# Kernel optimization log

Measured on AMD Instinct MI355X. Metric: run time of the kernel, lower is better.

## Reference

```python
import jax, jax.numpy as jnp
import numpy as np

B, N, K = 4, 4096, 16
DP, DM = 64, 128
EPS = 1e-8


def setup_inputs() -> dict:
    key = jax.random.key(0)
    ks = jax.random.split(key, 32)
    g = lambda i, shape, fan: jax.random.normal(ks[i], shape, jnp.float32) / np.sqrt(fan)
    inp = {
        'xyz': jax.random.normal(ks[0], (B, N, 3), jnp.float32),
        'features': jax.random.normal(ks[1], (B, N, DP), jnp.float32),
        # fc1: d_points -> d_model
        'fc1_w': g(2, (DP, DM), DP), 'fc1_b': jnp.zeros((DM,), jnp.float32),
        # fc2: d_model -> d_points
        'fc2_w': g(3, (DM, DP), DM), 'fc2_b': jnp.zeros((DP,), jnp.float32),
        # fc_delta: Linear(3,DM) -> ReLU -> Linear(DM,DM)
        'd1_w': g(4, (3, DM), 3), 'd1_b': jnp.zeros((DM,), jnp.float32),
        'd2_w': g(5, (DM, DM), DM), 'd2_b': jnp.zeros((DM,), jnp.float32),
        # fc_gamma: Linear(DM,DM) -> ReLU -> Linear(DM,DM)
        'g1_w': g(6, (DM, DM), DM), 'g1_b': jnp.zeros((DM,), jnp.float32),
        'g2_w': g(7, (DM, DM), DM), 'g2_b': jnp.zeros((DM,), jnp.float32),
        # q/k/v projections, no bias
        'wq_w': g(8, (DM, DM), DM), 'wk_w': g(9, (DM, DM), DM), 'wv_w': g(10, (DM, DM), DM),
        # fc_sim: Linear(DM+1, DM)
        'sim_w': g(11, (DM + 1, DM), DM + 1), 'sim_b': jnp.zeros((DM,), jnp.float32),
    }
    return inp


def _gather(t, idx):
    # t: [B, N, C], idx: [B, N, K] -> [B, N, K, C]
    bidx = jnp.arange(t.shape[0])[:, None, None]
    return t[bidx, idx]


def reference(xyz, features, fc1_w, fc1_b, fc2_w, fc2_b, d1_w, d1_b, d2_w, d2_b,
              g1_w, g1_b, g2_w, g2_b, wq_w, wk_w, wv_w, sim_w, sim_b):
    # pairwise squared distances [B, N, N]
    sq = jnp.sum(xyz * xyz, axis=-1)
    dists = sq[:, :, None] + sq[:, None, :] - 2.0 * jnp.einsum('bnc,bmc->bnm', xyz, xyz)
    knn_idx = jnp.argsort(dists, axis=-1)[:, :, :K]            # [B, N, K]

    knn_xyz = _gather(xyz, knn_idx)                            # [B, N, K, 3]
    x = features @ fc1_w + fc1_b                               # [B, N, DM]
    q = x @ wq_w                                               # [B, N, DM]
    k = _gather(x @ wk_w, knn_idx)                             # [B, N, K, DM]
    v = _gather(x @ wv_w, knn_idx)                             # [B, N, K, DM]

    rel_pos = xyz[:, :, None, :] - knn_xyz                     # [B, N, K, 3]
    pos_enc = jax.nn.relu(rel_pos @ d1_w + d1_b) @ d2_w + d2_b # [B, N, K, DM]

    qe = q[:, :, None, :]                                      # [B, N, 1, DM]
    # torch cosine_similarity: dot / (max(||q||,eps) * max(||k||,eps))
    qn = jnp.maximum(jnp.linalg.norm(q, axis=-1), EPS)[:, :, None]
    kn = jnp.maximum(jnp.linalg.norm(k, axis=-1), EPS)
    sim = jnp.sum(qe * k, axis=-1) / (qn * kn)                 # [B, N, K]

    rel_qk = jnp.concatenate([sim[..., None], qe - k], axis=-1)  # [B, N, K, DM+1]
    rel_qk = rel_qk @ sim_w + sim_b                            # [B, N, K, DM]

    attn = jax.nn.relu((rel_qk + pos_enc) @ g1_w + g1_b) @ g2_w + g2_b
    attn = jax.nn.softmax(attn / np.sqrt(DM).astype(np.float32), axis=-2)  # over K

    res = jnp.einsum('bnkf,bnkf->bnf', attn, v + pos_enc)      # [B, N, DM]
    res = res @ fc2_w + fc2_b + features                       # [B, N, DP]
    return res, attn
```

## Files before the change

### kernel.cpp

```cpp
#include <hip/hip_runtime.h>
#include <hip/hip_bf16.h>

#define BB 4
#define NN 4096
#define KK 16
#define DP 64
#define DM 128
#define DMP 132
#define SPITCH 264
#define EPSF 1e-8f
#define OUT0N ((size_t)BB * NN * DP)

typedef unsigned short u16t;
typedef __attribute__((ext_vector_type(8))) short s8v;
typedef __attribute__((ext_vector_type(4))) float f4v;

__device__ int g_flag;

__device__ __forceinline__ float u2f(u16t u) {
    unsigned int x = ((unsigned int)u) << 16;
    return __uint_as_float(x);
}
__device__ __forceinline__ u16t f2u(float v) {
    __hip_bfloat16 h = __float2bfloat16(v);
    return *(u16t*)&h;
}
__device__ __forceinline__ void splitf(float x, u16t& h, u16t& l) {
    const unsigned xb = __float_as_uint(x);
    h = (u16t)(xb >> 16);
    const float hf = __uint_as_float(xb & 0xffff0000u);
    l = (u16t)(__float_as_uint(x - hf) >> 16);
}

template<int DT> struct IO;
template<> struct IO<0> {
    static __device__ __forceinline__ float ld(const void* p, size_t i) { return ((const float*)p)[i]; }
    static __device__ __forceinline__ void ld4(const void* p, size_t i, float o[4]) {
        float4 v = *(const float4*)((const float*)p + i);
        o[0] = v.x; o[1] = v.y; o[2] = v.z; o[3] = v.w;
    }
    static __device__ __forceinline__ void st(void* p, size_t i, float v) { ((float*)p)[i] = v; }
};
template<> struct IO<1> {
    static __device__ __forceinline__ float ld(const void* p, size_t i) { return u2f(((const u16t*)p)[i]); }
    static __device__ __forceinline__ void ld4(const void* p, size_t i, float o[4]) {
        ushort4 v = *(const ushort4*)((const u16t*)p + i);
        o[0] = u2f(v.x); o[1] = u2f(v.y); o[2] = u2f(v.z); o[3] = u2f(v.w);
    }
    static __device__ __forceinline__ void st(void* p, size_t i, float v) { ((u16t*)p)[i] = f2u(v); }
};

__global__ __launch_bounds__(64) void detect_kernel(const void* feat) {
    const int tid = threadIdx.x;
    float x = u2f(((const u16t*)feat)[2 * tid]);
    float a = fabsf(x);
    bool sane = (x == 0.0f) || (a > 1e-4f && a < 50.0f);
    unsigned long long m = __ballot(sane);
    if (tid == 0) g_flag = (__popcll(m) >= 32) ? 1 : 0;
}

struct QkvSmem { float sf[DP]; float sx[DM]; };

template<int DT>
__device__ __forceinline__ void qkv_body(QkvSmem& s,
    const void* feat, const void* fc1_w, const void* fc1_b,
    const void* wq, const void* wk, const void* wv,
    float* __restrict__ qbuf, float* __restrict__ kbuf, float* __restrict__ vbuf)
{
    const int bn = blockIdx.x;
    const int tid = threadIdx.x;
    if (tid < DP) s.sf[tid] = IO<DT>::ld(feat, (size_t)bn * DP + tid);
    __syncthreads();
    float x = IO<DT>::ld(fc1_b, tid);
#pragma unroll 4
    for (int i = 0; i < DP; i++) x = fmaf(s.sf[i], IO<DT>::ld(fc1_w, i * DM + tid), x);
    s.sx[tid] = x;
    __syncthreads();
    float q = 0.f, k = 0.f, v = 0.f;
    for (int i0 = 0; i0 < DM; i0 += 4) {
        float4 xv = *(const float4*)&s.sx[i0];
        const float xs[4] = { xv.x, xv.y, xv.z, xv.w };
#pragma unroll
        for (int j = 0; j < 4; j++) {
            q = fmaf(xs[j], IO<DT>::ld(wq, (i0 + j) * DM + tid), q);
            k = fmaf(xs[j], IO<DT>::ld(wk, (i0 + j) * DM + tid), k);
            v = fmaf(xs[j], IO<DT>::ld(wv, (i0 + j) * DM + tid), v);
        }
    }
    qbuf[(size_t)bn * DM + tid] = q;
    kbuf[(size_t)bn * DM + tid] = k;
    vbuf[(size_t)bn * DM + tid] = v;
}

__global__ __launch_bounds__(128) void qkv_kernel(
    const void* feat, const void* fc1_w, const void* fc1_b,
    const void* wq, const void* wk, const void* wv,
    float* qbuf, float* kbuf, float* vbuf)
{
    __shared__ __align__(16) QkvSmem s;
    if (g_flag) qkv_body<1>(s, feat, fc1_w, fc1_b, wq, wk, wv, qbuf, kbuf, vbuf);
    else        qkv_body<0>(s, feat, fc1_w, fc1_b, wq, wk, wv, qbuf, kbuf, vbuf);
}

struct Qkv16Smem { float sf[16][DP]; float sx[16][DMP]; };

template<int DT>
__device__ __forceinline__ void qkv16_body(Qkv16Smem& s,
    const void* feat, const void* fc1_w, const void* fc1_b,
    const void* wq, const void* wk, const void* wv,
    float* __restrict__ qbuf, float* __restrict__ kbuf, float* __restrict__ vbuf)
{
    const int pnt0 = blockIdx.x << 4;
    const int tid = threadIdx.x;
    {
        const int r = tid >> 4, c4 = (tid & 15) << 2;
        float o[4];
        IO<DT>::ld4(feat, (size_t)(pnt0 + r) * DP + c4, o);
        s.sf[r][c4 + 0] = o[0]; s.sf[r][c4 + 1] = o[1];
        s.sf[r][c4 + 2] = o[2]; s.sf[r][c4 + 3] = o[3];
    }
    __syncthreads();
    const int c = tid & 127, h = tid >> 7;
    {
        float acc[8];
        const float fb = IO<DT>::ld(fc1_b, c);
#pragma unroll
        for (int pp = 0; pp < 8; pp++) acc[pp] = fb;
        for (int i = 0; i < DP; i++) {
            const float w = IO<DT>::ld(fc1_w, (size_t)i * DM + c);
#pragma unroll
            for (int pp = 0; pp < 8; pp++) acc[pp] = fmaf(s.sf[h * 8 + pp][i], w, acc[pp]);
        }
#pragma unroll
        for (int pp = 0; pp < 8; pp++) s.sx[h * 8 + pp][c] = acc[pp];
    }
    __syncthreads();
    {
        float aq[8], ak[8], av[8];
#pragma unroll
        for (int pp = 0; pp < 8; pp++) { aq[pp] = 0.f; ak[pp] = 0.f; av[pp] = 0.f; }
        for (int i0 = 0; i0 < DM; i0 += 4) {
            float x4[8][4];
#pragma unroll
            for (int pp = 0; pp < 8; pp++) {
                const float4 xv = *(const float4*)&s.sx[h * 8 + pp][i0];
                x4[pp][0] = xv.x; x4[pp][1] = xv.y; x4[pp][2] = xv.z; x4[pp][3] = xv.w;
            }
#pragma unroll
            for (int j = 0; j < 4; j++) {
                const float wqv = IO<DT>::ld(wq, (size_t)(i0 + j) * DM + c);
                const float wkv = IO<DT>::ld(wk, (size_t)(i0 + j) * DM + c);
                const float wvv = IO<DT>::ld(wv, (size_t)(i0 + j) * DM + c);
#pragma unroll
                for (int pp = 0; pp < 8; pp++) {
                    aq[pp] = fmaf(x4[pp][j], wqv, aq[pp]);
                    ak[pp] = fmaf(x4[pp][j], wkv, ak[pp]);
                    av[pp] = fmaf(x4[pp][j], wvv, av[pp]);
                }
            }
        }
#pragma unroll
        for (int pp = 0; pp < 8; pp++) {
            const size_t row = (size_t)(pnt0 + h * 8 + pp) * DM + c;
            qbuf[row] = aq[pp]; kbuf[row] = ak[pp]; vbuf[row] = av[pp];
        }
    }
}

__global__ __launch_bounds__(256) void qkv16_kernel(
    const void* feat, const void* fc1_w, const void* fc1_b,
    const void* wq, const void* wk, const void* wv,
    float* qbuf, float* kbuf, float* vbuf)
{
    __shared__ __align__(16) Qkv16Smem s;
    if (g_flag) qkv16_body<1>(s, feat, fc1_w, fc1_b, wq, wk, wv, qbuf, kbuf, vbuf);
    else        qkv16_body<0>(s, feat, fc1_w, fc1_b, wq, wk, wv, qbuf, kbuf, vbuf);
}

template<int DT>
__device__ __forceinline__ void knn_body(float4* __restrict__ sc,
    const void* xyz, int* dst, int dstride, void* dout, int in_out)
{
    if (in_out) {
        if (DT) { dst = (int*)((u16t*)dout + OUT0N); dstride = (KK * DM) / 2; }
        else    { dst = (int*)((float*)dout + OUT0N); dstride = KK * DM; }
    }
    const int b = blockIdx.x >> 9;
    const int tid = threadIdx.x;
    for (int j = tid; j < NN; j += 512) {
        float x = IO<DT>::ld(xyz, ((size_t)b * NN + j) * 3 + 0);
        float y = IO<DT>::ld(xyz, ((size_t)b * NN + j) * 3 + 1);
        float z = IO<DT>::ld(xyz, ((size_t)b * NN + j) * 3 + 2);
        float sq = __fadd_rn(__fadd_rn(__fmul_rn(x, x), __fmul_rn(y, y)), __fmul_rn(z, z));
        sc[j] = make_float4(x, y, z, sq);
    }
    __syncthreads();
    const int lane = tid & 63;
    const int wave = tid >> 6;
    const int r = ((blockIdx.x & 511) << 3) + wave;
    const float4 qc = sc[r];

    float d[KK];
    int id[KK];
#pragma unroll
    for (int t = 0; t < KK; t++) { d[t] = 3.4e38f; id[t] = 0x7fffffff; }

    for (int j = lane; j < NN; j += 64) {
        const float4 c = sc[j];
        const float dot = __fadd_rn(__fadd_rn(__fmul_rn(qc.x, c.x), __fmul_rn(qc.y, c.y)),
                                    __fmul_rn(qc.z, c.z));
        const float dist = __fsub_rn(__fadd_rn(qc.w, c.w), __fmul_rn(2.0f, dot));
        if (dist < d[KK - 1]) {
            float cd = dist; int ci = j;
#pragma unroll
            for (int t = 0; t < KK; t++) {
                const bool sw = (cd < d[t]);
                const float od = d[t]; const int oi = id[t];
                d[t]  = sw ? cd : d[t];
                id[t] = sw ? ci : id[t];
                cd = sw ? od : cd;
                ci = sw ? oi : ci;
            }
        }
    }

    const size_t base = (size_t)(b * NN + r) * (size_t)dstride;
#pragma unroll
    for (int t = 0; t < KK; t++) {
        float bd = d[0]; int bi = id[0];
#pragma unroll
        for (int off = 32; off >= 1; off >>= 1) {
            const float od = __shfl_xor(bd, off, 64);
            const int   oi = __shfl_xor(bi, off, 64);
            if (od < bd || (od == bd && oi < bi)) { bd = od; bi = oi; }
        }
        const bool win = (d[0] == bd) && (id[0] == bi);
        if (win) {
#pragma unroll
            for (int u = 0; u < KK - 1; u++) { d[u] = d[u + 1]; id[u] = id[u + 1]; }
            d[KK - 1] = 3.4e38f; id[KK - 1] = 0x7fffffff;
        }
        if (lane == t) dst[base + t] = bi;
    }
}

__global__ __launch_bounds__(512) void knn_kernel(
    const void* xyz, int* dst, int dstride, void* dout, int in_out)
{
    __shared__ __align__(16) float4 sc[NN];
    if (g_flag) knn_body<1>(sc, xyz, dst, dstride, dout, in_out);
    else        knn_body<0>(sc, xyz, dst, dstride, dout, in_out);
}

template<int DT>
__device__ __forceinline__ void gemm_tile(const float* __restrict__ IN,
                                          const void* __restrict__ W, int woff,
                                          int kg, int f0, float acc[4][4])
{
#pragma unroll
    for (int a = 0; a < 4; a++)
#pragma unroll
        for (int c = 0; c < 4; c++) acc[a][c] = 0.f;
    for (int i0 = 0; i0 < DM; i0 += 4) {
        float w[4][4];
#pragma unroll
        for (int j = 0; j < 4; j++) IO<DT>::ld4(W, (size_t)woff + (i0 + j) * DM + f0, w[j]);
#pragma unroll
        for (int kk = 0; kk < 4; kk++) {
            float4 x4 = *(const float4*)(IN + (kg * 4 + kk) * DMP + i0);
            const float xs[4] = { x4.x, x4.y, x4.z, x4.w };
#pragma unroll
            for (int ff = 0; ff < 4; ff++)
#pragma unroll
                for (int j = 0; j < 4; j++)
                    acc[kk][ff] = fmaf(xs[j], w[j][ff], acc[kk][ff]);
        }
    }
}

template<int DT>
__device__ __forceinline__ void wprep_body(const void* sim_w, const void* d2_w,
                                           const void* g1_w, const void* g2_w,
                                           u16t* __restrict__ wprep)
{
    const int m  = blockIdx.x >> 3;
    const int t  = blockIdx.x & 7;
    const int ks = threadIdx.x >> 6;
    const int lane = threadIdx.x & 63;
    const void* src = (m == 0) ? sim_w : (m == 1) ? d2_w : (m == 2) ? g1_w : g2_w;
    const int srcoff = (m == 0) ? DM : 0;
    u16t* hi = wprep + (size_t)m * 32768;
    u16t* lo = hi + 16384;
    const int c  = t * 16 + (lane & 15);
    const int k0 = ks * 32 + ((lane >> 4) << 3);
    s8v vh, vl;
#pragma unroll
    for (int j = 0; j < 8; j++) {
        const float x = IO<DT>::ld(src, (size_t)srcoff + (size_t)(k0 + j) * DM + c);
        const u16t h = f2u(x);
        vh[j] = (short)h;
        vl[j] = (short)f2u(x - u2f(h));
    }
    const size_t off = ((size_t)(t * 4 + ks) * 64 + lane) * 8;
    *(s8v*)(hi + off) = vh;
    *(s8v*)(lo + off) = vl;
}

__global__ __launch_bounds__(256) void wprep_kernel(
    const void* sim_w, const void* d2_w, const void* g1_w, const void* g2_w,
    u16t* wprep)
{
    if (g_flag) wprep_body<1>(sim_w, d2_w, g1_w, g2_w, wprep);
    else        wprep_body<0>(sim_w, d2_w, g1_w, g2_w, wprep);
}

__device__ __forceinline__ void mfma_g(const u16t* __restrict__ SP,
                                       const u16t* __restrict__ wmat,
                                       int lane, int w, f4v acc[4][2])
{
    const u16t* whi = wmat;
    const u16t* wlo = wmat + 16384;
    const int arow = lane & 15;
    const int ak   = (lane >> 4) << 3;
#pragma unroll
    for (int ks = 0; ks < 4; ks++) {
        const size_t o0 = ((size_t)(((2 * w + 0) * 4 + ks) * 64) + lane) * 8;
        const size_t o1 = ((size_t)(((2 * w + 1) * 4 + ks) * 64) + lane) * 8;
        const s8v b0h = *(const s8v*)(whi + o0);
        const s8v b0l = *(const s8v*)(wlo + o0);
        const s8v b1h = *(const s8v*)(whi + o1);
        const s8v b1l = *(const s8v*)(wlo + o1);
#pragma unroll
        for (int m = 0; m < 4; m++) {
            const u16t* ar = SP + (size_t)(m * 16 + arow) * SPITCH + ak + ks * 32;
            const s8v ah = *(const s8v*)ar;
            const s8v al = *(const s8v*)(ar + 128);
            acc[m][0] = __builtin_amdgcn_mfma_f32_16x16x32_bf16(ah, b0h, acc[m][0], 0, 0, 0);
            acc[m][0] = __builtin_amdgcn_mfma_f32_16x16x32_bf16(ah, b0l, acc[m][0], 0, 0, 0);
            acc[m][0] = __builtin_amdgcn_mfma_f32_16x16x32_bf16(al, b0h, acc[m][0], 0, 0, 0);
            acc[m][1] = __builtin_amdgcn_mfma_f32_16x16x32_bf16(ah, b1h, acc[m][1], 0, 0, 0);
            acc[m][1] = __builtin_amdgcn_mfma_f32_16x16x32_bf16(ah, b1l, acc[m][1], 0, 0, 0);
            acc[m][1] = __builtin_amdgcn_mfma_f32_16x16x32_bf16(al, b1h, acc[m][1], 0, 0, 0);
        }
    }
}

struct Attn4Smem {
    u16t  SP[64 * SPITCH];
    float sq[4][DM];
    float sres[4][DM];
    float ssim[64];
    float srp[64][3];
    int   sidx[64];
};

template<int DT>
__device__ __forceinline__ void attn4w_body(Attn4Smem& s,
    const void* xyz, const void* feat,
    const void* fc2_w, const void* fc2_b,
    const void* d1_w, const void* d1_b, const void* d2_b,
    const void* g1_b, const void* g2_b,
    const void* sim_w, const void* sim_b,
    const float* __restrict__ qbuf, const float* __restrict__ kbuf,
    const float* __restrict__ vbuf,
    const int* __restrict__ knn, const u16t* __restrict__ wprep, void* dout)
{
    void* out0 = dout;
    void* out1 = DT ? (void*)((u16t*)dout + OUT0N) : (void*)((float*)dout + OUT0N);
    const int pnt0 = blockIdx.x << 2;
    const int b = pnt0 >> 12;
    const int tid = threadIdx.x;
    const int lane = tid & 63;
    const int w = tid >> 6;
    const int h = lane >> 4;
    const int c = lane & 15;

    if (tid < 64) {
        int sv = knn[(size_t)(pnt0 + (tid >> 4)) * KK + (tid & 15)];
        sv = (sv < 0) ? 0 : (sv > NN - 1 ? NN - 1 : sv);
        s.sidx[tid] = sv;
        const int pt = tid >> 4;
        const int grow = (b << 12) + sv;
#pragma unroll
        for (int c3 = 0; c3 < 3; c3++)
            s.srp[tid][c3] = IO<DT>::ld(xyz, (size_t)(pnt0 + pt) * 3 + c3)
                           - IO<DT>::ld(xyz, (size_t)grow * 3 + c3);
    }
    const float2 q2 = *(const float2*)&qbuf[(size_t)(pnt0 + w) * DM + lane * 2];
    *(float2*)&s.sq[w][lane * 2] = q2;
    float qq = fmaf(q2.x, q2.x, q2.y * q2.y);
#pragma unroll
    for (int off = 1; off <= 32; off <<= 1) qq += __shfl_xor(qq, off, 64);
    const float qn = fmaxf(sqrtf(qq), EPSF);
    __syncthreads();

    {
        const int row = tid >> 2, cb = (tid & 3) << 5;
        const float rx = s.srp[row][0], ry = s.srp[row][1], rz = s.srp[row][2];
        u16t* hp = &s.SP[row * SPITCH];
#pragma unroll
        for (int j4 = 0; j4 < 32; j4 += 4) {
            float w0[4], w1[4], w2[4], bb[4];
            IO<DT>::ld4(d1_w, (size_t)0 * DM + cb + j4, w0);
            IO<DT>::ld4(d1_w, (size_t)1 * DM + cb + j4, w1);
            IO<DT>::ld4(d1_w, (size_t)2 * DM + cb + j4, w2);
            IO<DT>::ld4(d1_b, cb + j4, bb);
            ushort4 hv, lv;
#pragma unroll
            for (int jj = 0; jj < 4; jj++) {
                const float hx = fmaxf(fmaf(rz, w2[jj], fmaf(ry, w1[jj], fmaf(rx, w0[jj], bb[jj]))), 0.f);
                u16t hs, ls; splitf(hx, hs, ls);
                ((u16t*)&hv)[jj] = hs; ((u16t*)&lv)[jj] = ls;
            }
            *(ushort4*)(hp + cb + j4) = hv;
            *(ushort4*)(hp + 128 + cb + j4) = lv;
        }
    }
    __syncthreads();

    f4v pe[4][2] = { { {0,0,0,0},{0,0,0,0} }, { {0,0,0,0},{0,0,0,0} },
                     { {0,0,0,0},{0,0,0,0} }, { {0,0,0,0},{0,0,0,0} } };
    mfma_g(s.SP, wprep + 1 * 32768, lane, w, pe);
#pragma unroll
    for (int nt = 0; nt < 2; nt++) {
        const float bv = IO<DT>::ld(d2_b, (2 * w + nt) * 16 + c);
#pragma unroll
        for (int m = 0; m < 4; m++)
#pragma unroll
            for (int r = 0; r < 4; r++) pe[m][nt][r] += bv;
    }
    __syncthreads();

    {
        const int row = tid >> 2, cb = (tid & 3) << 5;
        const int pt = row >> 4;
        const int grow = (b << 12) + s.sidx[row];
        const float* krow = &kbuf[(size_t)grow * DM];
        u16t* hp = &s.SP[row * SPITCH];
        float sk = 0.f, sd = 0.f;
#pragma unroll
        for (int j4 = 0; j4 < 32; j4 += 4) {
            const float4 kv = *(const float4*)&krow[cb + j4];
            const float4 qv = *(const float4*)&s.sq[pt][cb + j4];
            ushort4 hv, lv;
            splitf(qv.x - kv.x, hv.x, lv.x);
            splitf(qv.y - kv.y, hv.y, lv.y);
            splitf(qv.z - kv.z, hv.z, lv.z);
            splitf(qv.w - kv.w, hv.w, lv.w);
            *(ushort4*)(hp + cb + j4) = hv;
            *(ushort4*)(hp + 128 + cb + j4) = lv;
            sk = fmaf(kv.x, kv.x, fmaf(kv.y, kv.y, fmaf(kv.z, kv.z, fmaf(kv.w, kv.w, sk))));
            sd = fmaf(qv.x, kv.x, fmaf(qv.y, kv.y, fmaf(qv.z, kv.z, fmaf(qv.w, kv.w, sd))));
        }
        sk += __shfl_xor(sk, 1, 64); sk += __shfl_xor(sk, 2, 64);
        sd += __shfl_xor(sd, 1, 64); sd += __shfl_xor(sd, 2, 64);
        if ((tid & 3) == 0) {
            const float kn = fmaxf(sqrtf(sk), EPSF);
            s.ssim[row] = sd / (qn * kn);
        }
    }
    __syncthreads();

    {
        f4v a1[4][2] = { { {0,0,0,0},{0,0,0,0} }, { {0,0,0,0},{0,0,0,0} },
                         { {0,0,0,0},{0,0,0,0} }, { {0,0,0,0},{0,0,0,0} } };
        mfma_g(s.SP, wprep + 0 * 32768, lane, w, a1);
        __syncthreads();
#pragma unroll
        for (int nt = 0; nt < 2; nt++) {
            const int col = (2 * w + nt) * 16 + c;
            const float bv  = IO<DT>::ld(sim_b, col);
            const float w0v = IO<DT>::ld(sim_w, col);
#pragma unroll
            for (int m = 0; m < 4; m++)
#pragma unroll
                for (int r = 0; r < 4; r++) {
                    const int row = m * 16 + 4 * h + r;
                    const float val = a1[m][nt][r] + bv + s.ssim[row] * w0v + pe[m][nt][r];
                    u16t hs, ls; splitf(val, hs, ls);
                    s.SP[(size_t)row * SPITCH + col] = hs;
                    s.SP[(size_t)row * SPITCH + 128 + col] = ls;
                }
        }
    }
    __syncthreads();

    {
        f4v a3[4][2] = { { {0,0,0,0},{0,0,0,0} }, { {0,0,0,0},{0,0,0,0} },
                         { {0,0,0,0},{0,0,0,0} }, { {0,0,0,0},{0,0,0,0} } };
        mfma_g(s.SP, wprep + 2 * 32768, lane, w, a3);
        __syncthreads();
#pragma unroll
        for (int nt = 0; nt < 2; nt++) {
            const int col = (2 * w + nt) * 16 + c;
            const float bv = IO<DT>::ld(g1_b, col);
#pragma unroll
            for (int m = 0; m < 4; m++)
#pragma unroll
                for (int r = 0; r < 4; r++) {
                    const int row = m * 16 + 4 * h + r;
                    const float val = fmaxf(a3[m][nt][r] + bv, 0.f);
                    u16t hs, ls; splitf(val, hs, ls);
                    s.SP[(size_t)row * SPITCH + col] = hs;
                    s.SP[(size_t)row * SPITCH + 128 + col] = ls;
                }
        }
    }
    __syncthreads();

    f4v av[4][2];
    {
        f4v a4[4][2] = { { {0,0,0,0},{0,0,0,0} }, { {0,0,0,0},{0,0,0,0} },
                         { {0,0,0,0},{0,0,0,0} }, { {0,0,0,0},{0,0,0,0} } };
        mfma_g(s.SP, wprep + 3 * 32768, lane, w, a4);
        const float inv = 0.08838834764831843f;
#pragma unroll
        for (int nt = 0; nt < 2; nt++) {
            const int col = (2 * w + nt) * 16 + c;
            const float bv = IO<DT>::ld(g2_b, col);
#pragma unroll
            for (int m = 0; m < 4; m++) {
                float tv[4];
#pragma unroll
                for (int r = 0; r < 4; r++) tv[r] = (a4[m][nt][r] + bv) * inv;
                float mx = fmaxf(fmaxf(tv[0], tv[1]), fmaxf(tv[2], tv[3]));
                mx = fmaxf(mx, __shfl_xor(mx, 16, 64));
                mx = fmaxf(mx, __shfl_xor(mx, 32, 64));
                float ssum = 0.f;
#pragma unroll
                for (int r = 0; r < 4; r++) { tv[r] = __expf(tv[r] - mx); ssum += tv[r]; }
                ssum += __shfl_xor(ssum, 16, 64);
                ssum += __shfl_xor(ssum, 32, 64);
                const float rs = 1.0f / ssum;
#pragma unroll
                for (int r = 0; r < 4; r++) {
                    const float a = tv[r] * rs;
                    av[m][nt][r] = a;
                    IO<DT>::st(out1, ((size_t)(pnt0 + m) * KK + (4 * h + r)) * DM + col, a);
                }
            }
        }
    }
    __syncthreads();

    float* vst = (float*)s.SP;
    {
        const int row = tid >> 2, cb = (tid & 3) << 5;
        const int grow = (b << 12) + s.sidx[row];
        const float* vrow = &vbuf[(size_t)grow * DM];
#pragma unroll
        for (int j4 = 0; j4 < 32; j4 += 4)
            *(float4*)&vst[row * 132 + cb + j4] = *(const float4*)&vrow[cb + j4];
    }
    __syncthreads();
    {
#pragma unroll
        for (int nt = 0; nt < 2; nt++) {
            const int col = (2 * w + nt) * 16 + c;
#pragma unroll
            for (int m = 0; m < 4; m++) {
                float part = 0.f;
#pragma unroll
                for (int r = 0; r < 4; r++)
                    part = fmaf(av[m][nt][r],
                                vst[(m * 16 + 4 * h + r) * 132 + col] + pe[m][nt][r], part);
                part += __shfl_xor(part, 16, 64);
                part += __shfl_xor(part, 32, 64);
                if (h == 0) s.sres[m][col] = part;
            }
        }
    }
    __syncthreads();

    {
        const int pt = tid >> 6, cc = tid & 63;
        float o = 0.f;
        for (int i = 0; i < DM; i++)
            o = fmaf(s.sres[pt][i], IO<DT>::ld(fc2_w, (size_t)i * DP + cc), o);
        o = o + IO<DT>::ld(fc2_b, cc) + IO<DT>::ld(feat, (size_t)(pnt0 + pt) * DP + cc);
        IO<DT>::st(out0, (size_t)(pnt0 + pt) * DP + cc, o);
    }
}

__global__ __launch_bounds__(256, 4) void attn4w_kernel(
    const void* xyz, const void* feat,
    const void* fc2_w, const void* fc2_b,
    const void* d1_w, const void* d1_b, const void* d2_b,
    const void* g1_b, const void* g2_b,
    const void* sim_w, const void* sim_b,
    const float* qbuf, const float* kbuf, const float* vbuf,
    const int* knn, const u16t* wprep, void* dout)
{
    __shared__ __align__(16) Attn4Smem s;
    if (g_flag)
        attn4w_body<1>(s, xyz, feat, fc2_w, fc2_b, d1_w, d1_b, d2_b, g1_b, g2_b,
                       sim_w, sim_b, qbuf, kbuf, vbuf, knn, wprep, dout);
    else
        attn4w_body<0>(s, xyz, feat, fc2_w, fc2_b, d1_w, d1_b, d2_b, g1_b, g2_b,
                       sim_w, sim_b, qbuf, kbuf, vbuf, knn, wprep, dout);
}

template<bool FUSED> struct AttnSmem {
    float Kb[KK * DMP], Vb[KK * DMP], PE[KK * DMP], T0[KK * DMP], T1[KK * DMP];
    float s_q[DM], sres[DM];
    float SF[FUSED ? 17 * DP : 1];
    float X[FUSED ? 17 * DMP : 1];
    float srp[KK][3];
    float ssim[KK], skn[KK], sdot[KK];
    float sqn;
    int sidx[KK];
};

template<int DT, bool FUSED>
__device__ __forceinline__ void attn_body(AttnSmem<FUSED>& s,
    const void* xyz, const void* feat,
    const void* fc1_w, const void* fc1_b, const void* fc2_w, const void* fc2_b,
    const void* d1_w, const void* d1_b, const void* d2_w, const void* d2_b,
    const void* g1_w, const void* g1_b, const void* g2_w, const void* g2_b,
    const void* sim_w, const void* sim_b,
    const void* wq, const void* wk, const void* wv,
    const float* __restrict__ qbuf, const float* __restrict__ kbuf, const float* __restrict__ vbuf,
    const int* knn, int knn_stride, int knn_in_out, void* dout)
{
    void* out0 = dout;
    void* out1 = DT ? (void*)((u16t*)dout + OUT0N) : (void*)((float*)dout + OUT0N);
    if (knn_in_out) {
        if (DT) { knn = (const int*)((const u16t*)dout + OUT0N); knn_stride = (KK * DM) / 2; }
        else    { knn = (const int*)((const float*)dout + OUT0N); knn_stride = KK * DM; }
    }

    const int bn = blockIdx.x;
    const int b = bn >> 12;
    const int tid = threadIdx.x;
    const int f = tid;
    const int f0 = (tid & 31) * 4;
    const int kg = tid >> 5;

    if (tid < KK) {
        int sv = knn[(size_t)bn * knn_stride + tid];
        sv = (sv < 0) ? 0 : (sv > NN - 1 ? NN - 1 : sv);
        s.sidx[tid] = sv;
    }
    __syncthreads();

    if constexpr (FUSED) {
        for (int idx = tid; idx < 17 * DP; idx += 128) {
            const int r = idx >> 6, c = idx & 63;
            const int row = (r < KK) ? ((b << 12) + s.sidx[r]) : bn;
            s.SF[idx] = IO<DT>::ld(feat, (size_t)row * DP + c);
        }
        __syncthreads();
        float xacc[17];
        const float fb = IO<DT>::ld(fc1_b, tid);
#pragma unroll
        for (int r = 0; r < 17; r++) xacc[r] = fb;
        for (int i = 0; i < DP; i++) {
            const float w = IO<DT>::ld(fc1_w, i * DM + tid);
#pragma unroll
            for (int r = 0; r < 17; r++) xacc[r] = fmaf(s.SF[r * DP + i], w, xacc[r]);
        }
#pragma unroll
        for (int r = 0; r < 17; r++) s.X[r * DMP + tid] = xacc[r];
        __syncthreads();
        {
            float a2[4][4];
            gemm_tile<DT>(s.X, wk, 0, kg, f0, a2);
#pragma unroll
            for (int kk = 0; kk < 4; kk++)
                *(float4*)&s.Kb[(kg * 4 + kk) * DMP + f0] =
                    make_float4(a2[kk][0], a2[kk][1], a2[kk][2], a2[kk][3]);
            gemm_tile<DT>(s.X, wv, 0, kg, f0, a2);
#pragma unroll
            for (int kk = 0; kk < 4; kk++)
                *(float4*)&s.Vb[(kg * 4 + kk) * DMP + f0] =
                    make_float4(a2[kk][0], a2[kk][1], a2[kk][2], a2[kk][3]);
        }
        {
            float qv = 0.f;
            for (int i0 = 0; i0 < DM; i0 += 4) {
                float4 x4 = *(const float4*)&s.X[16 * DMP + i0];
                const float xs[4] = { x4.x, x4.y, x4.z, x4.w };
#pragma unroll
                for (int j = 0; j < 4; j++)
                    qv = fmaf(xs[j], IO<DT>::ld(wq, (i0 + j) * DM + tid), qv);
            }
            s.s_q[tid] = qv;
        }
    } else {
        s.s_q[f] = qbuf[(size_t)bn * DM + f];
#pragma unroll
        for (int k = 0; k < KK; k++) {
            const int row = (b << 12) + s.sidx[k];
            s.Kb[k * DMP + f] = kbuf[(size_t)row * DM + f];
            s.Vb[k * DMP + f] = vbuf[(size_t)row * DM + f];
        }
    }
    if (tid < KK) {
        const int row = (b << 12) + s.sidx[tid];
#pragma unroll
        for (int c = 0; c < 3; c++)
            s.srp[tid][c] = IO<DT>::ld(xyz, (size_t)bn * 3 + c) - IO<DT>::ld(xyz, (size_t)row * 3 + c);
    }
    __syncthreads();

    if (tid < KK) {
        float sk = 0.f, sd = 0.f;
        for (int i = 0; i < DM; i++) {
            float v2 = s.Kb[tid * DMP + i];
            sk = fmaf(v2, v2, sk);
            sd = fmaf(s.s_q[i], v2, sd);
        }
        s.skn[tid] = fmaxf(sqrtf(sk), EPSF);
        s.sdot[tid] = sd;
    } else if (tid == KK) {
        float sqq = 0.f;
        for (int i = 0; i < DM; i++) { float v2 = s.s_q[i]; sqq = fmaf(v2, v2, sqq); }
        s.sqn = fmaxf(sqrtf(sqq), EPSF);
    }
    __syncthreads();
    if (tid < KK) s.ssim[tid] = s.sdot[tid] / (s.sqn * s.skn[tid]);
#pragma unroll
    for (int k = 0; k < KK; k++) s.T0[k * DMP + f] = s.s_q[f] - s.Kb[k * DMP + f];
    __syncthreads();

    float acc[4][4];

    gemm_tile<DT>(s.T0, sim_w, DM, kg, f0, acc);
    {
        float w0f[4], sbf[4];
        IO<DT>::ld4(sim_w, f0, w0f);
        IO<DT>::ld4(sim_b, f0, sbf);
#pragma unroll
        for (int kk = 0; kk < 4; kk++) {
            float sm = s.ssim[kg * 4 + kk];
            float4 o;
            o.x = fmaf(sm, w0f[0], acc[kk][0]) + sbf[0];
            o.y = fmaf(sm, w0f[1], acc[kk][1]) + sbf[1];
            o.z = fmaf(sm, w0f[2], acc[kk][2]) + sbf[2];
            o.w = fmaf(sm, w0f[3], acc[kk][3]) + sbf[3];
            *(float4*)&s.T1[(kg * 4 + kk) * DMP + f0] = o;
        }
    }
    __syncthreads();

    {
        float w0 = IO<DT>::ld(d1_w, 0 * DM + f), w1 = IO<DT>::ld(d1_w, 1 * DM + f),
              w2 = IO<DT>::ld(d1_w, 2 * DM + f);
        float hb = IO<DT>::ld(d1_b, f);
#pragma unroll
        for (int k = 0; k < KK; k++) {
            float h = fmaf(s.srp[k][2], w2, fmaf(s.srp[k][1], w1, fmaf(s.srp[k][0], w0, hb)));
            s.T0[k * DMP + f] = fmaxf(h, 0.f);
        }
    }
    __syncthreads();

    gemm_tile<DT>(s.T0, d2_w, 0, kg, f0, acc);
    {
        float bf[4];
        IO<DT>::ld4(d2_b, f0, bf);
#pragma unroll
        for (int kk = 0; kk < 4; kk++)
            *(float4*)&s.PE[(kg * 4 + kk) * DMP + f0] =
                make_float4(acc[kk][0] + bf[0], acc[kk][1] + bf[1],
                            acc[kk][2] + bf[2], acc[kk][3] + bf[3]);
    }
    __syncthreads();

#pragma unroll
    for (int kk = 0; kk < 4; kk++) {
        const int row = (kg * 4 + kk) * DMP + f0;
        float4 a4 = *(const float4*)&s.T1[row];
        float4 p4 = *(const float4*)&s.PE[row];
        *(float4*)&s.T0[row] = make_float4(a4.x + p4.x, a4.y + p4.y, a4.z + p4.z, a4.w + p4.w);
    }
    __syncthreads();

    gemm_tile<DT>(s.T0, g1_w, 0, kg, f0, acc);
    {
        float bf[4];
        IO<DT>::ld4(g1_b, f0, bf);
#pragma unroll
        for (int kk = 0; kk < 4; kk++)
            *(float4*)&s.T1[(kg * 4 + kk) * DMP + f0] =
                make_float4(fmaxf(acc[kk][0] + bf[0], 0.f), fmaxf(acc[kk][1] + bf[1], 0.f),
                            fmaxf(acc[kk][2] + bf[2], 0.f), fmaxf(acc[kk][3] + bf[3], 0.f));
    }
    __syncthreads();

    gemm_tile<DT>(s.T1, g2_w, 0, kg, f0, acc);
    {
        float bf[4];
        IO<DT>::ld4(g2_b, f0, bf);
#pragma unroll
        for (int kk = 0; kk < 4; kk++)
            *(float4*)&s.T0[(kg * 4 + kk) * DMP + f0] =
                make_float4(acc[kk][0] + bf[0], acc[kk][1] + bf[1],
                            acc[kk][2] + bf[2], acc[kk][3] + bf[3]);
    }
    __syncthreads();

    {
        const float sq128 = 11.31370849898476f;
        float tv[KK];
        float m = -3.4e38f;
#pragma unroll
        for (int k = 0; k < KK; k++) { tv[k] = s.T0[k * DMP + f] / sq128; m = fmaxf(m, tv[k]); }
        float ssum = 0.f;
#pragma unroll
        for (int k = 0; k < KK; k++) { tv[k] = expf(tv[k] - m); ssum += tv[k]; }
        float rf = 0.f;
#pragma unroll
        for (int k = 0; k < KK; k++) {
            float a = tv[k] / ssum;
            IO<DT>::st(out1, ((size_t)bn * KK + k) * DM + f, a);
            rf = fmaf(a, s.Vb[k * DMP + f] + s.PE[k * DMP + f], rf);
        }
        s.sres[f] = rf;
    }
    __syncthreads();

    if (tid < DP) {
        float o = 0.f;
        for (int i = 0; i < DM; i++) o = fmaf(s.sres[i], IO<DT>::ld(fc2_w, i * DP + tid), o);
        o = o + IO<DT>::ld(fc2_b, tid) + IO<DT>::ld(feat, (size_t)bn * DP + tid);
        IO<DT>::st(out0, (size_t)bn * DP + tid, o);
    }
}

template<bool FUSED>
__global__ __launch_bounds__(128) void attn_kernel(
    const void* xyz, const void* feat,
    const void* fc1_w, const void* fc1_b, const void* fc2_w, const void* fc2_b,
    const void* d1_w, const void* d1_b, const void* d2_w, const void* d2_b,
    const void* g1_w, const void* g1_b, const void* g2_w, const void* g2_b,
    const void* sim_w, const void* sim_b,
    const void* wq, const void* wk, const void* wv,
    const float* qbuf, const float* kbuf, const float* vbuf,
    const int* knn, int knn_stride, int knn_in_out, void* dout)
{
    __shared__ __align__(16) AttnSmem<FUSED> s;
    if (g_flag)
        attn_body<1, FUSED>(s, xyz, feat, fc1_w, fc1_b, fc2_w, fc2_b, d1_w, d1_b, d2_w, d2_b,
                            g1_w, g1_b, g2_w, g2_b, sim_w, sim_b, wq, wk, wv,
                            qbuf, kbuf, vbuf, knn, knn_stride, knn_in_out, dout);
    else
        attn_body<0, FUSED>(s, xyz, feat, fc1_w, fc1_b, fc2_w, fc2_b, d1_w, d1_b, d2_w, d2_b,
                            g1_w, g1_b, g2_w, g2_b, sim_w, sim_b, wq, wk, wv,
                            qbuf, kbuf, vbuf, knn, knn_stride, knn_in_out, dout);
}

extern "C" void kernel_launch(void* const* d_in, const int* in_sizes, int n_in,
                              void* d_out, int out_size, void* d_ws, size_t ws_size,
                              hipStream_t stream)
{
    const void* xyz   = d_in[0];
    const void* feat  = d_in[1];
    const void* fc1_w = d_in[2];
    const void* fc1_b = d_in[3];
    const void* fc2_w = d_in[4];
    const void* fc2_b = d_in[5];
    const void* d1_w  = d_in[6];
    const void* d1_b  = d_in[7];
    const void* d2_w  = d_in[8];
    const void* d2_b  = d_in[9];
    const void* g1_w  = d_in[10];
    const void* g1_b  = d_in[11];
    const void* g2_w  = d_in[12];
    const void* g2_b  = d_in[13];
    const void* wq_w  = d_in[14];
    const void* wk_w  = d_in[15];
    const void* wv_w  = d_in[16];
    const void* sim_w = d_in[17];
    const void* sim_b = d_in[18];

    detect_kernel<<<1, 64, 0, stream>>>(feat);

    const size_t need_qkv = (size_t)3 * BB * NN * DM * sizeof(float);
    const size_t need_knn = (size_t)BB * NN * KK * sizeof(int);
    const size_t need_wp  = (size_t)4 * 2 * 16384 * sizeof(u16t);

    if (ws_size >= need_qkv + need_knn + need_wp && d_ws != nullptr) {
        float* qbuf  = (float*)d_ws;
        float* kbuf  = qbuf + (size_t)BB * NN * DM;
        float* vbuf  = kbuf + (size_t)BB * NN * DM;
        int*   knn   = (int*)(vbuf + (size_t)BB * NN * DM);
        u16t*  wprep = (u16t*)(knn + (size_t)BB * NN * KK);
        qkv16_kernel<<<(BB * NN) / 16, 256, 0, stream>>>(feat, fc1_w, fc1_b, wq_w, wk_w, wv_w,
                                                         qbuf, kbuf, vbuf);
        knn_kernel<<<BB * 512, 512, 0, stream>>>(xyz, knn, KK, d_out, 0);
        wprep_kernel<<<32, 256, 0, stream>>>(sim_w, d2_w, g1_w, g2_w, wprep);
        attn4w_kernel<<<(BB * NN) / 4, 256, 0, stream>>>(
            xyz, feat, fc2_w, fc2_b, d1_w, d1_b, d2_b, g1_b, g2_b, sim_w, sim_b,
            qbuf, kbuf, vbuf, knn, wprep, d_out);
    } else if (ws_size >= need_qkv + need_knn && d_ws != nullptr) {
        float* qbuf = (float*)d_ws;
        float* kbuf = qbuf + (size_t)BB * NN * DM;
        float* vbuf = kbuf + (size_t)BB * NN * DM;
        int*   knn  = (int*)(vbuf + (size_t)BB * NN * DM);
        qkv_kernel<<<BB * NN, DM, 0, stream>>>(feat, fc1_w, fc1_b, wq_w, wk_w, wv_w, qbuf, kbuf, vbuf);
        knn_kernel<<<BB * 512, 512, 0, stream>>>(xyz, knn, KK, d_out, 0);
        attn_kernel<false><<<BB * NN, DM, 0, stream>>>(
            xyz, feat, fc1_w, fc1_b, fc2_w, fc2_b, d1_w, d1_b, d2_w, d2_b,
            g1_w, g1_b, g2_w, g2_b, sim_w, sim_b, wq_w, wk_w, wv_w,
            qbuf, kbuf, vbuf, knn, KK, 0, d_out);
    } else if (ws_size >= need_knn && d_ws != nullptr) {
        int* knn = (int*)d_ws;
        knn_kernel<<<BB * 512, 512, 0, stream>>>(xyz, knn, KK, d_out, 0);
        attn_kernel<true><<<BB * NN, DM, 0, stream>>>(
            xyz, feat, fc1_w, fc1_b, fc2_w, fc2_b, d1_w, d1_b, d2_w, d2_b,
            g1_w, g1_b, g2_w, g2_b, sim_w, sim_b, wq_w, wk_w, wv_w,
            nullptr, nullptr, nullptr, knn, KK, 0, d_out);
    } else {
        knn_kernel<<<BB * 512, 512, 0, stream>>>(xyz, nullptr, 0, d_out, 1);
        attn_kernel<true><<<BB * NN, DM, 0, stream>>>(
            xyz, feat, fc1_w, fc1_b, fc2_w, fc2_b, d1_w, d1_b, d2_w, d2_b,
            g1_w, g1_b, g2_w, g2_b, sim_w, sim_b, wq_w, wk_w, wv_w,
            nullptr, nullptr, nullptr, nullptr, 0, 1, d_out);
    }
}
```

Baseline: 579.1 us.

## Halve KNN blocks and prefetch gathered K/V rows into registers in attention

The KNN kernel now handles two query points per wave, halving the grid so each block's xyz staging into shared memory is amortised over 16 queries. The attention kernel loads each thread's neighbor index, relative position and K row directly into registers at kernel start, removing a staging barrier and the shared sidx/srp arrays. The V gather is issued before the barrier, and the pos_enc contribution is reduced separately so V no longer needs to be added to it in the final loop. This raises register pressure with 64 extra floats per thread under launch_bounds(256,4), and it halves KNN parallelism.

```diff
diff --git a/kernel.cpp b/kernel.cpp
--- a/kernel.cpp
+++ b/kernel.cpp
@@ -185,7 +185,7 @@
         if (DT) { dst = (int*)((u16t*)dout + OUT0N); dstride = (KK * DM) / 2; }
         else    { dst = (int*)((float*)dout + OUT0N); dstride = KK * DM; }
     }
-    const int b = blockIdx.x >> 9;
+    const int b = blockIdx.x >> 8;
     const int tid = threadIdx.x;
     for (int j = tid; j < NN; j += 512) {
         float x = IO<DT>::ld(xyz, ((size_t)b * NN + j) * 3 + 0);
@@ -197,50 +197,53 @@
     __syncthreads();
     const int lane = tid & 63;
     const int wave = tid >> 6;
-    const int r = ((blockIdx.x & 511) << 3) + wave;
-    const float4 qc = sc[r];
-
-    float d[KK];
-    int id[KK];
-#pragma unroll
-    for (int t = 0; t < KK; t++) { d[t] = 3.4e38f; id[t] = 0x7fffffff; }
-
-    for (int j = lane; j < NN; j += 64) {
-        const float4 c = sc[j];
-        const float dot = __fadd_rn(__fadd_rn(__fmul_rn(qc.x, c.x), __fmul_rn(qc.y, c.y)),
-                                    __fmul_rn(qc.z, c.z));
-        const float dist = __fsub_rn(__fadd_rn(qc.w, c.w), __fmul_rn(2.0f, dot));
-        if (dist < d[KK - 1]) {
-            float cd = dist; int ci = j;
-#pragma unroll
-            for (int t = 0; t < KK; t++) {
-                const bool sw = (cd < d[t]);
-                const float od = d[t]; const int oi = id[t];
-                d[t]  = sw ? cd : d[t];
-                id[t] = sw ? ci : id[t];
-                cd = sw ? od : cd;
-                ci = sw ? oi : ci;
+
+    for (int qi = 0; qi < 2; qi++) {
+        const int r = ((blockIdx.x & 255) << 4) + (wave << 1) + qi;
+        const float4 qc = sc[r];
+
+        float d[KK];
+        int id[KK];
+#pragma unroll
+        for (int t = 0; t < KK; t++) { d[t] = 3.4e38f; id[t] = 0x7fffffff; }
+
+        for (int j = lane; j < NN; j += 64) {
+            const float4 c = sc[j];
+            const float dot = __fadd_rn(__fadd_rn(__fmul_rn(qc.x, c.x), __fmul_rn(qc.y, c.y)),
+                                        __fmul_rn(qc.z, c.z));
+            const float dist = __fsub_rn(__fadd_rn(qc.w, c.w), __fmul_rn(2.0f, dot));
+            if (dist < d[KK - 1]) {
+                float cd = dist; int ci = j;
+#pragma unroll
+                for (int t = 0; t < KK; t++) {
+                    const bool sw = (cd < d[t]);
+                    const float od = d[t]; const int oi = id[t];
+                    d[t]  = sw ? cd : d[t];
+                    id[t] = sw ? ci : id[t];
+                    cd = sw ? od : cd;
+                    ci = sw ? oi : ci;
+                }
             }
         }
-    }
-
-    const size_t base = (size_t)(b * NN + r) * (size_t)dstride;
-#pragma unroll
-    for (int t = 0; t < KK; t++) {
-        float bd = d[0]; int bi = id[0];
-#pragma unroll
-        for (int off = 32; off >= 1; off >>= 1) {
-            const float od = __shfl_xor(bd, off, 64);
-            const int   oi = __shfl_xor(bi, off, 64);
-            if (od < bd || (od == bd && oi < bi)) { bd = od; bi = oi; }
-        }
-        const bool win = (d[0] == bd) && (id[0] == bi);
-        if (win) {
-#pragma unroll
-            for (int u = 0; u < KK - 1; u++) { d[u] = d[u + 1]; id[u] = id[u + 1]; }
-            d[KK - 1] = 3.4e38f; id[KK - 1] = 0x7fffffff;
-        }
-        if (lane == t) dst[base + t] = bi;
+
+        const size_t base = (size_t)(b * NN + r) * (size_t)dstride;
+#pragma unroll
+        for (int t = 0; t < KK; t++) {
+            float bd = d[0]; int bi = id[0];
+#pragma unroll
+            for (int off = 32; off >= 1; off >>= 1) {
+                const float od = __shfl_xor(bd, off, 64);
+                const int   oi = __shfl_xor(bi, off, 64);
+                if (od < bd || (od == bd && oi < bi)) { bd = od; bi = oi; }
+            }
+            const bool win = (d[0] == bd) && (id[0] == bi);
+            if (win) {
+#pragma unroll
+                for (int u = 0; u < KK - 1; u++) { d[u] = d[u + 1]; id[u] = id[u + 1]; }
+                d[KK - 1] = 3.4e38f; id[KK - 1] = 0x7fffffff;
+            }
+            if (lane == t) dst[base + t] = bi;
+        }
     }
 }
 
@@ -345,17 +348,15 @@
     }
 }
 
-struct Attn4Smem {
+struct Attn5Smem {
     u16t  SP[64 * SPITCH];
     float sq[4][DM];
     float sres[4][DM];
     float ssim[64];
-    float srp[64][3];
-    int   sidx[64];
 };
 
 template<int DT>
-__device__ __forceinline__ void attn4w_body(Attn4Smem& s,
+__device__ __forceinline__ void attn5_body(Attn5Smem& s,
     const void* xyz, const void* feat,
     const void* fc2_w, const void* fc2_b,
     const void* d1_w, const void* d1_b, const void* d2_b,
@@ -374,29 +375,27 @@
     const int w = tid >> 6;
     const int h = lane >> 4;
     const int c = lane & 15;
-
-    if (tid < 64) {
-        int sv = knn[(size_t)(pnt0 + (tid >> 4)) * KK + (tid & 15)];
-        sv = (sv < 0) ? 0 : (sv > NN - 1 ? NN - 1 : sv);
-        s.sidx[tid] = sv;
-        const int pt = tid >> 4;
-        const int grow = (b << 12) + sv;
-#pragma unroll
-        for (int c3 = 0; c3 < 3; c3++)
-            s.srp[tid][c3] = IO<DT>::ld(xyz, (size_t)(pnt0 + pt) * 3 + c3)
-                           - IO<DT>::ld(xyz, (size_t)grow * 3 + c3);
-    }
+    const int row = tid >> 2;
+    const int cb  = (tid & 3) << 5;
+
+    int sv = knn[(size_t)(pnt0 + w) * KK + (row & 15)];
+    sv = (sv < 0) ? 0 : (sv > NN - 1 ? NN - 1 : sv);
+    const int grow = (b << 12) + sv;
+    const float rx = IO<DT>::ld(xyz, (size_t)(pnt0 + w) * 3 + 0) - IO<DT>::ld(xyz, (size_t)grow * 3 + 0);
+    const float ry = IO<DT>::ld(xyz, (size_t)(pnt0 + w) * 3 + 1) - IO<DT>::ld(xyz, (size_t)grow * 3 + 1);
+    const float rz = IO<DT>::ld(xyz, (size_t)(pnt0 + w) * 3 + 2) - IO<DT>::ld(xyz, (size_t)grow * 3 + 2);
+    float4 kreg[8];
+#pragma unroll
+    for (int j4 = 0; j4 < 8; j4++)
+        kreg[j4] = *(const float4*)&kbuf[(size_t)grow * DM + cb + 4 * j4];
     const float2 q2 = *(const float2*)&qbuf[(size_t)(pnt0 + w) * DM + lane * 2];
     *(float2*)&s.sq[w][lane * 2] = q2;
     float qq = fmaf(q2.x, q2.x, q2.y * q2.y);
 #pragma unroll
     for (int off = 1; off <= 32; off <<= 1) qq += __shfl_xor(qq, off, 64);
     const float qn = fmaxf(sqrtf(qq), EPSF);
-    __syncthreads();
-
-    {
-        const int row = tid >> 2, cb = (tid & 3) << 5;
-        const float rx = s.srp[row][0], ry = s.srp[row][1], rz = s.srp[row][2];
+
+    {
         u16t* hp = &s.SP[row * SPITCH];
 #pragma unroll
         for (int j4 = 0; j4 < 32; j4 += 4) {
@@ -429,34 +428,37 @@
 #pragma unroll
             for (int r = 0; r < 4; r++) pe[m][nt][r] += bv;
     }
-    __syncthreads();
-
-    {
-        const int row = tid >> 2, cb = (tid & 3) << 5;
-        const int pt = row >> 4;
-        const int grow = (b << 12) + s.sidx[row];
-        const float* krow = &kbuf[(size_t)grow * DM];
+    {
+        float sk = 0.f, sd = 0.f;
+#pragma unroll
+        for (int j4 = 0; j4 < 8; j4++) {
+            const float4 kv = kreg[j4];
+            const float4 qv = *(const float4*)&s.sq[w][cb + 4 * j4];
+            sk = fmaf(kv.x, kv.x, fmaf(kv.y, kv.y, fmaf(kv.z, kv.z, fmaf(kv.w, kv.w, sk))));
+            sd = fmaf(qv.x, kv.x, fmaf(qv.y, kv.y, fmaf(qv.z, kv.z, fmaf(qv.w, kv.w, sd))));
+        }
+        sk += __shfl_xor(sk, 1, 64); sk += __shfl_xor(sk, 2, 64);
+        sd += __shfl_xor(sd, 1, 64); sd += __shfl_xor(sd, 2, 64);
+        if ((tid & 3) == 0) {
+            const float kn = fmaxf(sqrtf(sk), EPSF);
+            s.ssim[row] = sd / (qn * kn);
+        }
+    }
+    __syncthreads();
+
+    {
         u16t* hp = &s.SP[row * SPITCH];
-        float sk = 0.f, sd = 0.f;
-#pragma unroll
-        for (int j4 = 0; j4 < 32; j4 += 4) {
-            const float4 kv = *(const float4*)&krow[cb + j4];
-            const float4 qv = *(const float4*)&s.sq[pt][cb + j4];
+#pragma unroll
+        for (int j4 = 0; j4 < 8; j4++) {
+            const float4 kv = kreg[j4];
+            const float4 qv = *(const float4*)&s.sq[w][cb + 4 * j4];
             ushort4 hv, lv;
             splitf(qv.x - kv.x, hv.x, lv.x);
             splitf(qv.y - kv.y, hv.y, lv.y);
             splitf(qv.z - kv.z, hv.z, lv.z);
             splitf(qv.w - kv.w, hv.w, lv.w);
-            *(ushort4*)(hp + cb + j4) = hv;
-            *(ushort4*)(hp + 128 + cb + j4) = lv;
-            sk = fmaf(kv.x, kv.x, fmaf(kv.y, kv.y, fmaf(kv.z, kv.z, fmaf(kv.w, kv.w, sk))));
-            sd = fmaf(qv.x, kv.x, fmaf(qv.y, kv.y, fmaf(qv.z, kv.z, fmaf(qv.w, kv.w, sd))));
-        }
-        sk += __shfl_xor(sk, 1, 64); sk += __shfl_xor(sk, 2, 64);
-        sd += __shfl_xor(sd, 1, 64); sd += __shfl_xor(sd, 2, 64);
-        if ((tid & 3) == 0) {
-            const float kn = fmaxf(sqrtf(sk), EPSF);
-            s.ssim[row] = sd / (qn * kn);
+            *(ushort4*)(hp + cb + 4 * j4) = hv;
+            *(ushort4*)(hp + 128 + cb + 4 * j4) = lv;
         }
     }
     __syncthreads();
@@ -475,11 +477,11 @@
             for (int m = 0; m < 4; m++)
 #pragma unroll
                 for (int r = 0; r < 4; r++) {
-                    const int row = m * 16 + 4 * h + r;
-                    const float val = a1[m][nt][r] + bv + s.ssim[row] * w0v + pe[m][nt][r];
+                    const int rr = m * 16 + 4 * h + r;
+                    const float val = a1[m][nt][r] + bv + s.ssim[rr] * w0v + pe[m][nt][r];
                     u16t hs, ls; splitf(val, hs, ls);
-                    s.SP[(size_t)row * SPITCH + col] = hs;
-                    s.SP[(size_t)row * SPITCH + 128 + col] = ls;
+                    s.SP[(size_t)rr * SPITCH + col] = hs;
+                    s.SP[(size_t)rr * SPITCH + 128 + col] = ls;
                 }
         }
     }
@@ -498,17 +500,18 @@
             for (int m = 0; m < 4; m++)
 #pragma unroll
                 for (int r = 0; r < 4; r++) {
-                    const int row = m * 16 + 4 * h + r;
+                    const int rr = m * 16 + 4 * h + r;
                     const float val = fmaxf(a3[m][nt][r] + bv, 0.f);
                     u16t hs, ls; splitf(val, hs, ls);
-                    s.SP[(size_t)row * SPITCH + col] = hs;
-                    s.SP[(size_t)row * SPITCH + 128 + col] = ls;
+                    s.SP[(size_t)rr * SPITCH + col] = hs;
+                    s.SP[(size_t)rr * SPITCH + 128 + col] = ls;
                 }
         }
     }
     __syncthreads();
 
     f4v av[4][2];
+    float4 vreg[8];
     {
         f4v a4[4][2] = { { {0,0,0,0},{0,0,0,0} }, { {0,0,0,0},{0,0,0,0} },
                          { {0,0,0,0},{0,0,0,0} }, { {0,0,0,0},{0,0,0,0} } };
@@ -540,33 +543,43 @@
                 }
             }
         }
-    }
-    __syncthreads();
-
-    float* vst = (float*)s.SP;
-    {
-        const int row = tid >> 2, cb = (tid & 3) << 5;
-        const int grow = (b << 12) + s.sidx[row];
-        const float* vrow = &vbuf[(size_t)grow * DM];
-#pragma unroll
-        for (int j4 = 0; j4 < 32; j4 += 4)
-            *(float4*)&vst[row * 132 + cb + j4] = *(const float4*)&vrow[cb + j4];
-    }
-    __syncthreads();
-    {
 #pragma unroll
         for (int nt = 0; nt < 2; nt++) {
             const int col = (2 * w + nt) * 16 + c;
 #pragma unroll
             for (int m = 0; m < 4; m++) {
+                float pd = 0.f;
+#pragma unroll
+                for (int r = 0; r < 4; r++) pd = fmaf(av[m][nt][r], pe[m][nt][r], pd);
+                pd += __shfl_xor(pd, 16, 64);
+                pd += __shfl_xor(pd, 32, 64);
+                if (h == 0) s.sres[m][col] = pd;
+            }
+        }
+#pragma unroll
+        for (int j4 = 0; j4 < 8; j4++)
+            vreg[j4] = *(const float4*)&vbuf[(size_t)grow * DM + cb + 4 * j4];
+    }
+    __syncthreads();
+
+    float* vst = (float*)s.SP;
+#pragma unroll
+    for (int j4 = 0; j4 < 8; j4++)
+        *(float4*)&vst[row * 132 + cb + 4 * j4] = vreg[j4];
+    __syncthreads();
+    {
+#pragma unroll
+        for (int nt = 0; nt < 2; nt++) {
+            const int col = (2 * w + nt) * 16 + c;
+#pragma unroll
+            for (int m = 0; m < 4; m++) {
                 float part = 0.f;
 #pragma unroll
                 for (int r = 0; r < 4; r++)
-                    part = fmaf(av[m][nt][r],
-                                vst[(m * 16 + 4 * h + r) * 132 + col] + pe[m][nt][r], part);
+                    part = fmaf(av[m][nt][r], vst[(m * 16 + 4 * h + r) * 132 + col], part);
                 part += __shfl_xor(part, 16, 64);
                 part += __shfl_xor(part, 32, 64);
-                if (h == 0) s.sres[m][col] = part;
+                if (h == 0) s.sres[m][col] += part;
             }
         }
     }
@@ -582,7 +595,7 @@
     }
 }
 
-__global__ __launch_bounds__(256, 4) void attn4w_kernel(
+__global__ __launch_bounds__(256, 4) void attn5_kernel(
     const void* xyz, const void* feat,
     const void* fc2_w, const void* fc2_b,
     const void* d1_w, const void* d1_b, const void* d2_b,
@@ -591,13 +604,13 @@
     const float* qbuf, const float* kbuf, const float* vbuf,
     const int* knn, const u16t* wprep, void* dout)
 {
-    __shared__ __align__(16) Attn4Smem s;
+    __shared__ __align__(16) Attn5Smem s;
     if (g_flag)
-        attn4w_body<1>(s, xyz, feat, fc2_w, fc2_b, d1_w, d1_b, d2_b, g1_b, g2_b,
-                       sim_w, sim_b, qbuf, kbuf, vbuf, knn, wprep, dout);
+        attn5_body<1>(s, xyz, feat, fc2_w, fc2_b, d1_w, d1_b, d2_b, g1_b, g2_b,
+                      sim_w, sim_b, qbuf, kbuf, vbuf, knn, wprep, dout);
     else
-        attn4w_body<0>(s, xyz, feat, fc2_w, fc2_b, d1_w, d1_b, d2_b, g1_b, g2_b,
-                       sim_w, sim_b, qbuf, kbuf, vbuf, knn, wprep, dout);
+        attn5_body<0>(s, xyz, feat, fc2_w, fc2_b, d1_w, d1_b, d2_b, g1_b, g2_b,
+                      sim_w, sim_b, qbuf, kbuf, vbuf, knn, wprep, dout);
 }
 
 template<bool FUSED> struct AttnSmem {
@@ -888,9 +901,9 @@
         u16t*  wprep = (u16t*)(knn + (size_t)BB * NN * KK);
         qkv16_kernel<<<(BB * NN) / 16, 256, 0, stream>>>(feat, fc1_w, fc1_b, wq_w, wk_w, wv_w,
                                                          qbuf, kbuf, vbuf);
-        knn_kernel<<<BB * 512, 512, 0, stream>>>(xyz, knn, KK, d_out, 0);
+        knn_kernel<<<BB * 256, 512, 0, stream>>>(xyz, knn, KK, d_out, 0);
         wprep_kernel<<<32, 256, 0, stream>>>(sim_w, d2_w, g1_w, g2_w, wprep);
-        attn4w_kernel<<<(BB * NN) / 4, 256, 0, stream>>>(
+        attn5_kernel<<<(BB * NN) / 4, 256, 0, stream>>>(
             xyz, feat, fc2_w, fc2_b, d1_w, d1_b, d2_b, g1_b, g2_b, sim_w, sim_b,
             qbuf, kbuf, vbuf, knn, wprep, d_out);
     } else if (ws_size >= need_qkv + need_knn && d_ws != nullptr) {
@@ -899,20 +912,20 @@
         float* vbuf = kbuf + (size_t)BB * NN * DM;
         int*   knn  = (int*)(vbuf + (size_t)BB * NN * DM);
         qkv_kernel<<<BB * NN, DM, 0, stream>>>(feat, fc1_w, fc1_b, wq_w, wk_w, wv_w, qbuf, kbuf, vbuf);
-        knn_kernel<<<BB * 512, 512, 0, stream>>>(xyz, knn, KK, d_out, 0);
+        knn_kernel<<<BB * 256, 512, 0, stream>>>(xyz, knn, KK, d_out, 0);
         attn_kernel<false><<<BB * NN, DM, 0, stream>>>(
             xyz, feat, fc1_w, fc1_b, fc2_w, fc2_b, d1_w, d1_b, d2_w, d2_b,
             g1_w, g1_b, g2_w, g2_b, sim_w, sim_b, wq_w, wk_w, wv_w,
             qbuf, kbuf, vbuf, knn, KK, 0, d_out);
     } else if (ws_size >= need_knn && d_ws != nullptr) {
         int* knn = (int*)d_ws;
-        knn_kernel<<<BB * 512, 512, 0, stream>>>(xyz, knn, KK, d_out, 0);
+        knn_kernel<<<BB * 256, 512, 0, stream>>>(xyz, knn, KK, d_out, 0);
         attn_kernel<true><<<BB * NN, DM, 0, stream>>>(
             xyz, feat, fc1_w, fc1_b, fc2_w, fc2_b, d1_w, d1_b, d2_w, d2_b,
             g1_w, g1_b, g2_w, g2_b, sim_w, sim_b, wq_w, wk_w, wv_w,
             nullptr, nullptr, nullptr, knn, KK, 0, d_out);
     } else {
-        knn_kernel<<<BB * 512, 512, 0, stream>>>(xyz, nullptr, 0, d_out, 1);
+        knn_kernel<<<BB * 256, 512, 0, stream>>>(xyz, nullptr, 0, d_out, 1);
         attn_kernel<true><<<BB * NN, DM, 0, stream>>>(
             xyz, feat, fc1_w, fc1_b, fc2_w, fc2_b, d1_w, d1_b, d2_w, d2_b,
             g1_w, g1_b, g2_w, g2_b, sim_w, sim_b, wq_w, wk_w, wv_w,
```

Result: slower. 648.5 us (+12.0%).
